# Kernel tuning notes

Hardware: AMD Instinct MI355X
Metric: run time of the kernel (lower is better)

The kernel has to match this reference:

```python
import jax, jax.numpy as jnp
import numpy as np

N_EMBD = 1024
N_HEAD = 16
HEAD_DIM = N_EMBD // N_HEAD
BLOCK = 2048
BATCH = 2


def setup_inputs() -> dict:
    key = jax.random.key(0)
    ks = jax.random.split(key, 6)
    s_in = 1.0 / np.sqrt(N_EMBD)
    s_hd = 1.0 / np.sqrt(N_EMBD)  # fan-in of c_proj1 is n_head*head_dim = n_embd
    return {
        "x": jax.random.normal(ks[0], (BATCH, BLOCK, N_EMBD), jnp.float32),
        "wq": jax.random.normal(ks[1], (N_EMBD, N_HEAD, HEAD_DIM), jnp.float32) * s_in,
        "wk": jax.random.normal(ks[2], (N_EMBD, N_HEAD, HEAD_DIM), jnp.float32) * s_in,
        "wv": jax.random.normal(ks[3], (N_EMBD, N_HEAD, HEAD_DIM), jnp.float32) * s_in,
        "wp1": jax.random.normal(ks[4], (N_HEAD, HEAD_DIM, N_EMBD), jnp.float32) * s_hd,
        "wp2": jax.random.normal(ks[5], (N_EMBD, N_EMBD), jnp.float32) * s_in,
    }


def reference(x, wq, wk, wv, wp1, wp2):
    # QKV projections: DenseGeneral(features=(H, D), axis=-1), no bias
    q = jnp.einsum('btc,chd->bthd', x, wq)
    k = jnp.einsum('btc,chd->bthd', x, wk)
    v = jnp.einsum('btc,chd->bthd', x, wv)
    scale = HEAD_DIM ** (-0.5)
    wei = jnp.einsum('bqhd,bkhd->bhqk', q, k) * scale  # [B,H,T,T]
    tril = jnp.tril(jnp.ones((BLOCK, BLOCK), dtype=bool))
    wei = jnp.where(tril, wei, -jnp.inf)
    wei = jax.nn.softmax(wei, axis=-1)
    att = jnp.einsum('bhqk,bkhd->bqhd', wei, v)  # [B,T,H,D]
    # c_proj1: DenseGeneral over (-2,-1) -> contract (H,D)
    y = jnp.einsum('bqhd,hdc->bqc', att, wp1)
    # c_proj2: Dense
    out = jnp.einsum('bqc,ce->bqe', y, wp2)
    return out
```

## Files before the change

### kernel.cpp

```cpp
#include <hip/hip_runtime.h>
#include <hip/hip_bf16.h>
#include <stdint.h>

typedef __bf16 bf16;
typedef __bf16 bf16x4 __attribute__((ext_vector_type(4)));
typedef __bf16 bf16x8 __attribute__((ext_vector_type(8)));
typedef float  f32x4  __attribute__((ext_vector_type(4)));

#define MFMA16(a,b,c) __builtin_amdgcn_mfma_f32_16x16x32_bf16((a),(b),(c),0,0,0)

#define TSEQ 2048
#define NE   1024
#define NE3  3072
#define NH   16
#define HD   64
#define MTOK 4096

#if defined(__has_builtin) && __has_builtin(__builtin_amdgcn_exp2f)
#define EXP2F(x) __builtin_amdgcn_exp2f(x)
#else
__device__ __forceinline__ float exp2_fast(float x) {
  float r; asm("v_exp_f32 %0, %1" : "=v"(r) : "v"(x)); return r;
}
#define EXP2F(x) exp2_fast(x)
#endif

__device__ __forceinline__ void gl_lds16(const bf16* g, bf16* l) {
  __builtin_amdgcn_global_load_lds(
      (const __attribute__((address_space(1))) void*)g,
      (__attribute__((address_space(3))) void*)l,
      16, 0, 0);
}

__global__ void k_cast(const float* __restrict__ in, bf16* __restrict__ out, int n4) {
  int i = blockIdx.x * blockDim.x + threadIdx.x;
  if (i < n4) {
    float4 v = reinterpret_cast<const float4*>(in)[i];
    bf16x4 o = { (bf16)v.x, (bf16)v.y, (bf16)v.z, (bf16)v.w };
    reinterpret_cast<bf16x4*>(out)[i] = o;
  }
}

__global__ void k_transpose_all(const float* __restrict__ wq, const float* __restrict__ wk,
                                const float* __restrict__ wv, const float* __restrict__ wp2,
                                const float* __restrict__ wp1,
                                bf16* __restrict__ W3T, bf16* __restrict__ Wp2T,
                                bf16* __restrict__ Wp1b) {
  __shared__ float tile[64][65];
  const int z = blockIdx.z;
  const int r0 = blockIdx.y * 64, c0 = blockIdx.x * 64;
  const int lc = threadIdx.x & 63, lr0 = threadIdx.x >> 6;
  if (z == 4) {
#pragma unroll
    for (int i = 0; i < 16; ++i) {
      int lr = i*4 + lr0;
      Wp1b[(size_t)(r0 + lr)*1024 + c0 + lc] = (bf16)wp1[(size_t)(r0 + lr)*1024 + c0 + lc];
    }
    return;
  }
  const float* in = (z == 0) ? wq : (z == 1) ? wk : (z == 2) ? wv : wp2;
  bf16* out = (z < 3) ? (W3T + (size_t)z * 1024 * 1024) : Wp2T;
#pragma unroll
  for (int i = 0; i < 16; ++i) {
    int lr = i*4 + lr0;
    tile[lr][lc] = in[(size_t)(r0 + lr) * 1024 + (c0 + lc)];
  }
  __syncthreads();
#pragma unroll
  for (int i = 0; i < 16; ++i) {
    int lr = i*4 + lr0;
    out[(size_t)(c0 + lr) * 1024 + (r0 + lc)] = (bf16)tile[lc][lr];
  }
}

__global__ void k_transpose_v(const bf16* __restrict__ V, bf16* __restrict__ Vt) {
  __shared__ bf16 tile[64][65];
  const int b = blockIdx.z, h = blockIdx.y, t0 = blockIdx.x * 64;
  const int lc = threadIdx.x & 63, lr0 = threadIdx.x >> 6;
#pragma unroll
  for (int i = 0; i < 16; ++i) {
    int lr = i*4 + lr0;
    tile[lr][lc] = V[(size_t)(b*TSEQ + t0 + lr)*NE3 + h*HD + lc];
  }
  __syncthreads();
#pragma unroll
  for (int i = 0; i < 16; ++i) {
    int lr = i*4 + lr0;
    Vt[((size_t)(b*NH + h)*HD + lr)*TSEQ + t0 + lc] = tile[lc][lr];
  }
}

template<int BN, typename OutT>
__global__ __launch_bounds__(256) void k_gemm_bt(const bf16* __restrict__ A,
                                                 const bf16* __restrict__ Bt,
                                                 OutT* __restrict__ C,
                                                 const int M, const int N, const int K) {
  constexpr int NC = BN / 32;
  __shared__ bf16 As[2][128*32];
  __shared__ bf16 Bs[2][BN*32];
  const int tid  = threadIdx.x;
  const int lane = tid & 63;
  const int wave = tid >> 6;
  const int wr = (wave >> 1) * 64;
  const int wc = (wave & 1) * (BN/2);
  const int l15 = lane & 15;
  const int l4  = lane >> 4;

  const int nwg = gridDim.x * gridDim.y;
  int id = blockIdx.y * gridDim.x + blockIdx.x;
  id = (id & 7) * (nwg >> 3) + (id >> 3);
  const int bm = (id / gridDim.x) * 128;
  const int bn = (id % gridDim.x) * BN;

  const int srow = tid >> 2;
  const int scol = ((tid & 3) ^ ((tid >> 3) & 3)) * 8;
  const bf16* ag = A  + (size_t)(bm + srow) * K + scol;
  const bf16* bg = Bt + (size_t)(bn + srow) * K + scol;
  const int kx = (l4 ^ ((l15 >> 1) & 3)) * 8;

  f32x4 acc[4][NC] = {};

  auto stage = [&](int buf, int k0) {
    bf16* al = As[buf] + tid * 8;
    bf16* bl = Bs[buf] + tid * 8;
    gl_lds16(ag + k0,                   al);
    gl_lds16(ag + k0 + (size_t)64 * K,  al + 64*32);
    gl_lds16(bg + k0,                   bl);
    if (BN == 128) gl_lds16(bg + k0 + (size_t)64 * K, bl + 64*32);
  };

  stage(0, 0);
  __syncthreads();
  int cur = 0;
  for (int k0 = 0; k0 < K; k0 += 32) {
    if (k0 + 32 < K) stage(cur ^ 1, k0 + 32);
    bf16x8 af[4], bfr[NC];
#pragma unroll
    for (int m = 0; m < 4; ++m)
      af[m] = *reinterpret_cast<const bf16x8*>(&As[cur][(wr + m*16 + l15)*32 + kx]);
#pragma unroll
    for (int n = 0; n < NC; ++n)
      bfr[n] = *reinterpret_cast<const bf16x8*>(&Bs[cur][(wc + n*16 + l15)*32 + kx]);
#pragma unroll
    for (int m = 0; m < 4; ++m)
#pragma unroll
      for (int n = 0; n < NC; ++n)
        acc[m][n] = MFMA16(af[m], bfr[n], acc[m][n]);
    __syncthreads();
    cur ^= 1;
  }

#pragma unroll
  for (int m = 0; m < 4; ++m) {
    const int row = bm + wr + m*16 + l4*4;
#pragma unroll
    for (int n = 0; n < NC; ++n) {
      const int col = bn + wc + n*16 + l15;
#pragma unroll
      for (int r = 0; r < 4; ++r)
        C[(size_t)(row + r) * N + col] = (OutT)acc[m][n][r];
    }
  }
}

__global__ __launch_bounds__(512) void k_attn(const bf16* __restrict__ QKV,
                                              const bf16* __restrict__ Vt,
                                              bf16* __restrict__ O) {
  __shared__ bf16 KVs[3][16384];
  __shared__ bf16 Ps[8][4*16*32];

  const int tid  = threadIdx.x;
  const int lane = tid & 63;
  const int wave = tid >> 6;
  const int l15 = lane & 15;
  const int l4  = lane >> 4;

  const int x  = blockIdx.x;
  const int p  = x >> 5;
  const int bh = x & 31;
  const int b  = bh >> 4, h = bh & 15;

  const bf16* Qb = QKV + (size_t)b*TSEQ*NE3 +        h*HD;
  const bf16* Kb = QKV + (size_t)b*TSEQ*NE3 + 1024 + h*HD;
  const bf16* Vb = Vt  + (size_t)bh*HD*TSEQ;
  bf16* Pw = Ps[wave];

  const float SC = 0.125f * 1.44269504f;
  const int swz = (l4 ^ ((l15 >> 1) & 3)) * 8;
  const int key = (l15 >> 1) & 3;

  const int krow = tid >> 2;
  const int kg   = (tid & 3) ^ ((krow >> 1) & 3);
  const int vd   = (tid >> 2) & 63;
  const int vg   = (tid & 3) ^ ((vd >> 1) & 3);
  const int vp0  = tid >> 8;

  auto tileOf = [&](int j) { return (j <= p) ? j : (j - p - 1); };

  auto stage = [&](int buf, int t) {
    bf16* kb = &KVs[buf][0];
    bf16* vb = &KVs[buf][8192];
#pragma unroll
    for (int kk = 0; kk < 2; ++kk)
      gl_lds16(&Kb[(size_t)(t*128 + krow)*NE3 + kk*32 + kg*8], kb + kk*4096 + tid*8);
#pragma unroll
    for (int kk = 0; kk < 2; ++kk) {
      const int ksv = kk*2 + vp0;
      gl_lds16(&Vb[(size_t)vd*TSEQ + t*128 + ksv*32 + vg*8],  vb + kk*4096 + tid*8);
    }
  };

  stage(0, tileOf(0));
  stage(1, tileOf(1));
  int i = 0;

  for (int ci = 0; ci < 2; ++ci) {
    const int c  = ci ? (15 - p) : p;
    const int qw = c*128 + wave*16;

    bf16x8 qf[2];
#pragma unroll
    for (int ks = 0; ks < 2; ++ks) {
      bf16x8 qv = *reinterpret_cast<const bf16x8*>(
          &Qb[(size_t)(qw + l15)*NE3 + ks*32 + l4*8]);
#pragma unroll
      for (int j = 0; j < 8; ++j) qv[j] = (bf16)((float)qv[j] * SC);
      qf[ks] = qv;
    }

    f32x4 ot[4] = {};
    float m_run = -1e30f;
    float l_part = 0.f;

    for (int t = 0; t <= c; ++t, ++i) {
      asm volatile("s_waitcnt vmcnt(4)" ::: "memory");
      __builtin_amdgcn_sched_barrier(0);
      __builtin_amdgcn_s_barrier();
      __builtin_amdgcn_sched_barrier(0);
      const int j2 = (i + 2 <= 16) ? (i + 2) : 16;
      stage((i + 2) % 3, tileOf(j2));
      __builtin_amdgcn_sched_barrier(0);

      const bf16* kbuf = &KVs[i % 3][0];
      const bf16* vbuf = &KVs[i % 3][8192];

      f32x4 st[8];
#pragma unroll
      for (int kvf = 0; kvf < 8; ++kvf) {
        st[kvf] = f32x4{0.f, 0.f, 0.f, 0.f};
        const int row = kvf*16 + l15;
#pragma unroll
        for (int ks = 0; ks < 2; ++ks) {
          bf16x8 kf = *reinterpret_cast<const bf16x8*>(&kbuf[ks*4096 + row*32 + swz]);
          st[kvf] = MFMA16(kf, qf[ks], st[kvf]);
        }
      }

      if (t == c) {
#pragma unroll
        for (int kvf = 0; kvf < 8; ++kvf)
#pragma unroll
          for (int r = 0; r < 4; ++r)
            if (kvf*16 + l4*4 + r > wave*16 + l15) st[kvf][r] = -1e30f;
      }

      float mx = st[0][0];
#pragma unroll
      for (int kvf = 0; kvf < 8; ++kvf)
#pragma unroll
        for (int r = 0; r < 4; ++r) mx = fmaxf(mx, st[kvf][r]);
      mx = fmaxf(mx, __shfl_xor(mx, 16));
      mx = fmaxf(mx, __shfl_xor(mx, 32));

      if (__any(mx > m_run + 8.f)) {
        const float mnew = fmaxf(m_run, mx);
        const float corr = EXP2F(m_run - mnew);
        l_part *= corr;
#pragma unroll
        for (int n2 = 0; n2 < 4; ++n2) ot[n2] *= corr;
        m_run = mnew;
      }

      float rs = 0.f;
#pragma unroll
      for (int kvf = 0; kvf < 8; ++kvf) {
        bf16x4 pk;
#pragma unroll
        for (int r = 0; r < 4; ++r) {
          const float pv = EXP2F(st[kvf][r] - m_run);
          rs += pv;
          pk[r] = (bf16)pv;
        }
        const int gp = (((kvf & 1)*2 + (l4 >> 1)) ^ key);
        *reinterpret_cast<bf16x4*>(
            &Pw[(kvf>>1)*512 + l15*32 + gp*8 + (l4 & 1)*4]) = pk;
      }
      l_part += rs;

      bf16x8 pa[4];
#pragma unroll
      for (int ksv = 0; ksv < 4; ++ksv)
        pa[ksv] = *reinterpret_cast<const bf16x8*>(&Pw[ksv*512 + l15*32 + swz]);
#pragma unroll
      for (int n2 = 0; n2 < 4; ++n2) {
        const int vrow = n2*16 + l15;
#pragma unroll
        for (int ksv = 0; ksv < 4; ++ksv) {
          bf16x8 vf = *reinterpret_cast<const bf16x8*>(&vbuf[ksv*2048 + vrow*32 + swz]);
          ot[n2] = MFMA16(vf, pa[ksv], ot[n2]);
        }
      }
    }

    float l = l_part;
    l += __shfl_xor(l, 16);
    l += __shfl_xor(l, 32);
    const float rl = 1.f / l;
    const size_t row = (size_t)(b*TSEQ + qw + l15);
#pragma unroll
    for (int n2 = 0; n2 < 4; ++n2) {
      bf16x4 ov;
#pragma unroll
      for (int r = 0; r < 4; ++r) ov[r] = (bf16)(ot[n2][r] * rl);
      *reinterpret_cast<bf16x4*>(&O[row*NE + h*HD + n2*16 + l4*4]) = ov;
    }
  }
}

extern "C" void kernel_launch(void* const* d_in, const int* in_sizes, int n_in,
                              void* d_out, int out_size, void* d_ws, size_t ws_size,
                              hipStream_t stream) {
  const float* x   = (const float*)d_in[0];
  const float* wq  = (const float*)d_in[1];
  const float* wk  = (const float*)d_in[2];
  const float* wv  = (const float*)d_in[3];
  const float* wp1 = (const float*)d_in[4];
  const float* wp2 = (const float*)d_in[5];
  float* out = (float*)d_out;

  char* ws = (char*)d_ws;
  const size_t MB = 1024ull * 1024ull;
  bf16* xb   = (bf16*)(ws + 0*MB);
  bf16* W3T  = (bf16*)(ws + 8*MB);
  bf16* wp1b = (bf16*)(ws + 14*MB);
  bf16* wp2T = (bf16*)(ws + 16*MB);
  bf16* WcT  = (bf16*)(ws + 18*MB);
  bf16* QKVb = (bf16*)(ws + 20*MB);
  bf16* Vtb  = (bf16*)(ws + 44*MB);
  bf16* attb = (bf16*)(ws + 52*MB);

  k_cast<<<4096, 256, 0, stream>>>(x, xb, MTOK*NE/4);
  k_transpose_all<<<dim3(16, 16, 5), 256, 0, stream>>>(wq, wk, wv, wp2, wp1,
                                                       W3T, wp2T, wp1b);

  k_gemm_bt<64, bf16><<<dim3(16, 8), 256, 0, stream>>>(wp2T, wp1b, WcT, 1024, 1024, 1024);

  k_gemm_bt<128, bf16><<<dim3(24, 32), 256, 0, stream>>>(xb, W3T, QKVb, MTOK, NE3, NE);

  k_transpose_v<<<dim3(TSEQ/64, NH, 2), 256, 0, stream>>>(QKVb + 2048, Vtb);

  k_attn<<<dim3(256), 512, 0, stream>>>(QKVb, Vtb, attb);

  k_gemm_bt<128, float><<<dim3(8, 32), 256, 0, stream>>>(attb, WcT, out, MTOK, NE, NE);
}
```

Measured before the change: 129.5 us.

## Rewrite attention with 32x32 MFMA, register-resident P via permlane swap

The attention kernel moves from 16x16x32 to 32x32x16 bf16 MFMA with 4 waves of 32 query rows each, instead of 8 waves of 16. Softmax probabilities are now packed with v_cvt_pk_bf16 and rearranged across lanes with v_permlane32_swap, so they feed the PV MFMA straight from registers instead of going through an LDS scratch buffer. It also skips fully masked key blocks on the diagonal tile and changes the K/V LDS swizzle to match the new layout. This removes LDS traffic and some masked work, but halves the waves per block and raises register pressure.

```diff
diff --git a/kernel.cpp b/kernel.cpp
--- a/kernel.cpp
+++ b/kernel.cpp
@@ -6,8 +6,10 @@
 typedef __bf16 bf16x4 __attribute__((ext_vector_type(4)));
 typedef __bf16 bf16x8 __attribute__((ext_vector_type(8)));
 typedef float  f32x4  __attribute__((ext_vector_type(4)));
+typedef float  f32x16 __attribute__((ext_vector_type(16)));
 
 #define MFMA16(a,b,c) __builtin_amdgcn_mfma_f32_16x16x32_bf16((a),(b),(c),0,0,0)
+#define MFMA32(a,b,c) __builtin_amdgcn_mfma_f32_32x32x16_bf16((a),(b),(c),0,0,0)
 
 #define TSEQ 2048
 #define NE   1024
@@ -24,6 +26,15 @@
 }
 #define EXP2F(x) exp2_fast(x)
 #endif
+
+__device__ __forceinline__ unsigned cvt_pk_bf16(float lo, float hi) {
+  unsigned r;
+  asm("v_cvt_pk_bf16_f32 %0, %1, %2" : "=v"(r) : "v"(lo), "v"(hi));
+  return r;
+}
+__device__ __forceinline__ void permlane32_swap(unsigned& a, unsigned& b) {
+  asm("v_permlane32_swap_b32 %0, %1" : "+v"(a), "+v"(b));
+}
 
 __device__ __forceinline__ void gl_lds16(const bf16* g, bf16* l) {
   __builtin_amdgcn_global_load_lds(
@@ -163,17 +174,16 @@
   }
 }
 
-__global__ __launch_bounds__(512) void k_attn(const bf16* __restrict__ QKV,
+__global__ __launch_bounds__(256) void k_attn(const bf16* __restrict__ QKV,
                                               const bf16* __restrict__ Vt,
                                               bf16* __restrict__ O) {
   __shared__ bf16 KVs[3][16384];
-  __shared__ bf16 Ps[8][4*16*32];
 
   const int tid  = threadIdx.x;
   const int lane = tid & 63;
   const int wave = tid >> 6;
-  const int l15 = lane & 15;
-  const int l4  = lane >> 4;
+  const int l31 = lane & 31;
+  const int l32 = lane >> 5;
 
   const int x  = blockIdx.x;
   const int p  = x >> 5;
@@ -183,17 +193,13 @@
   const bf16* Qb = QKV + (size_t)b*TSEQ*NE3 +        h*HD;
   const bf16* Kb = QKV + (size_t)b*TSEQ*NE3 + 1024 + h*HD;
   const bf16* Vb = Vt  + (size_t)bh*HD*TSEQ;
-  bf16* Pw = Ps[wave];
 
   const float SC = 0.125f * 1.44269504f;
-  const int swz = (l4 ^ ((l15 >> 1) & 3)) * 8;
-  const int key = (l15 >> 1) & 3;
-
-  const int krow = tid >> 2;
-  const int kg   = (tid & 3) ^ ((krow >> 1) & 3);
-  const int vd   = (tid >> 2) & 63;
-  const int vg   = (tid & 3) ^ ((vd >> 1) & 3);
-  const int vp0  = tid >> 8;
+
+  const int krow0 = tid >> 3;
+  const int kgd   = tid & 7;
+  const int vrow0 = tid >> 4;
+  const int vgd   = tid & 15;
 
   auto tileOf = [&](int j) { return (j <= p) ? j : (j - p - 1); };
 
@@ -201,12 +207,16 @@
     bf16* kb = &KVs[buf][0];
     bf16* vb = &KVs[buf][8192];
 #pragma unroll
-    for (int kk = 0; kk < 2; ++kk)
-      gl_lds16(&Kb[(size_t)(t*128 + krow)*NE3 + kk*32 + kg*8], kb + kk*4096 + tid*8);
-#pragma unroll
-    for (int kk = 0; kk < 2; ++kk) {
-      const int ksv = kk*2 + vp0;
-      gl_lds16(&Vb[(size_t)vd*TSEQ + t*128 + ksv*32 + vg*8],  vb + kk*4096 + tid*8);
+    for (int rr = 0; rr < 4; ++rr) {
+      const int r = rr*32 + krow0;
+      const int gs = kgd ^ (r & 7);
+      gl_lds16(&Kb[(size_t)(t*128 + r)*NE3 + gs*8], kb + rr*2048 + tid*8);
+    }
+#pragma unroll
+    for (int rr = 0; rr < 4; ++rr) {
+      const int d = rr*16 + vrow0;
+      const int gs = vgd ^ (d & 15);
+      gl_lds16(&Vb[(size_t)d*TSEQ + t*128 + gs*8], vb + rr*2048 + tid*8);
     }
   };
 
@@ -216,24 +226,24 @@
 
   for (int ci = 0; ci < 2; ++ci) {
     const int c  = ci ? (15 - p) : p;
-    const int qw = c*128 + wave*16;
-
-    bf16x8 qf[2];
-#pragma unroll
-    for (int ks = 0; ks < 2; ++ks) {
+    const int qw = c*128 + wave*32;
+
+    bf16x8 qf[4];
+#pragma unroll
+    for (int ks = 0; ks < 4; ++ks) {
       bf16x8 qv = *reinterpret_cast<const bf16x8*>(
-          &Qb[(size_t)(qw + l15)*NE3 + ks*32 + l4*8]);
+          &Qb[(size_t)(qw + l31)*NE3 + ks*16 + l32*8]);
 #pragma unroll
       for (int j = 0; j < 8; ++j) qv[j] = (bf16)((float)qv[j] * SC);
       qf[ks] = qv;
     }
 
-    f32x4 ot[4] = {};
+    f32x16 ot[2] = {};
     float m_run = -1e30f;
     float l_part = 0.f;
 
     for (int t = 0; t <= c; ++t, ++i) {
-      asm volatile("s_waitcnt vmcnt(4)" ::: "memory");
+      asm volatile("s_waitcnt vmcnt(8)" ::: "memory");
       __builtin_amdgcn_sched_barrier(0);
       __builtin_amdgcn_s_barrier();
       __builtin_amdgcn_sched_barrier(0);
@@ -244,32 +254,38 @@
       const bf16* kbuf = &KVs[i % 3][0];
       const bf16* vbuf = &KVs[i % 3][8192];
 
-      f32x4 st[8];
-#pragma unroll
-      for (int kvf = 0; kvf < 8; ++kvf) {
-        st[kvf] = f32x4{0.f, 0.f, 0.f, 0.f};
-        const int row = kvf*16 + l15;
-#pragma unroll
-        for (int ks = 0; ks < 2; ++ks) {
-          bf16x8 kf = *reinterpret_cast<const bf16x8*>(&kbuf[ks*4096 + row*32 + swz]);
-          st[kvf] = MFMA16(kf, qf[ks], st[kvf]);
+      const int nkb = (t == c) ? (wave + 1) : 4;
+
+      f32x16 st[4];
+#pragma unroll
+      for (int kb = 0; kb < 4; ++kb) {
+        if (kb >= nkb) continue;
+        f32x16 acc = {};
+        const int rk = kb*32 + l31;
+#pragma unroll
+        for (int ks = 0; ks < 4; ++ks) {
+          const int g = (2*ks + l32) ^ (rk & 7);
+          bf16x8 kf = *reinterpret_cast<const bf16x8*>(&kbuf[rk*64 + g*8]);
+          acc = MFMA32(kf, qf[ks], acc);
         }
+        st[kb] = acc;
       }
 
       if (t == c) {
 #pragma unroll
-        for (int kvf = 0; kvf < 8; ++kvf)
-#pragma unroll
-          for (int r = 0; r < 4; ++r)
-            if (kvf*16 + l4*4 + r > wave*16 + l15) st[kvf][r] = -1e30f;
-      }
-
-      float mx = st[0][0];
-#pragma unroll
-      for (int kvf = 0; kvf < 8; ++kvf)
-#pragma unroll
-        for (int r = 0; r < 4; ++r) mx = fmaxf(mx, st[kvf][r]);
-      mx = fmaxf(mx, __shfl_xor(mx, 16));
+        for (int r = 0; r < 16; ++r) {
+          const int o = (r & 3) + 8*(r >> 2) + 4*l32;
+          if (o > l31) st[wave][r] = -1e30f;
+        }
+      }
+
+      float mx = -1e30f;
+#pragma unroll
+      for (int kb = 0; kb < 4; ++kb) {
+        if (kb >= nkb) continue;
+#pragma unroll
+        for (int r = 0; r < 16; ++r) mx = fmaxf(mx, st[kb][r]);
+      }
       mx = fmaxf(mx, __shfl_xor(mx, 32));
 
       if (__any(mx > m_run + 8.f)) {
@@ -277,53 +293,67 @@
         const float corr = EXP2F(m_run - mnew);
         l_part *= corr;
 #pragma unroll
-        for (int n2 = 0; n2 < 4; ++n2) ot[n2] *= corr;
+        for (int dbl = 0; dbl < 2; ++dbl) ot[dbl] *= corr;
         m_run = mnew;
       }
 
-      float rs = 0.f;
-#pragma unroll
-      for (int kvf = 0; kvf < 8; ++kvf) {
-        bf16x4 pk;
-#pragma unroll
-        for (int r = 0; r < 4; ++r) {
-          const float pv = EXP2F(st[kvf][r] - m_run);
-          rs += pv;
-          pk[r] = (bf16)pv;
+      bf16x8 pb[8];
+#pragma unroll
+      for (int kb = 0; kb < 4; ++kb) {
+        if (kb >= nkb) continue;
+        float pv[16];
+#pragma unroll
+        for (int r = 0; r < 16; ++r) {
+          pv[r] = EXP2F(st[kb][r] - m_run);
+          l_part += pv[r];
         }
-        const int gp = (((kvf & 1)*2 + (l4 >> 1)) ^ key);
-        *reinterpret_cast<bf16x4*>(
-            &Pw[(kvf>>1)*512 + l15*32 + gp*8 + (l4 & 1)*4]) = pk;
-      }
-      l_part += rs;
-
-      bf16x8 pa[4];
-#pragma unroll
-      for (int ksv = 0; ksv < 4; ++ksv)
-        pa[ksv] = *reinterpret_cast<const bf16x8*>(&Pw[ksv*512 + l15*32 + swz]);
-#pragma unroll
-      for (int n2 = 0; n2 < 4; ++n2) {
-        const int vrow = n2*16 + l15;
-#pragma unroll
-        for (int ksv = 0; ksv < 4; ++ksv) {
-          bf16x8 vf = *reinterpret_cast<const bf16x8*>(&vbuf[ksv*2048 + vrow*32 + swz]);
-          ot[n2] = MFMA16(vf, pa[ksv], ot[n2]);
+        unsigned c01 = cvt_pk_bf16(pv[0],  pv[1]);
+        unsigned c23 = cvt_pk_bf16(pv[2],  pv[3]);
+        unsigned c45 = cvt_pk_bf16(pv[4],  pv[5]);
+        unsigned c67 = cvt_pk_bf16(pv[6],  pv[7]);
+        unsigned c89 = cvt_pk_bf16(pv[8],  pv[9]);
+        unsigned cAB = cvt_pk_bf16(pv[10], pv[11]);
+        unsigned cCD = cvt_pk_bf16(pv[12], pv[13]);
+        unsigned cEF = cvt_pk_bf16(pv[14], pv[15]);
+        permlane32_swap(c01, c45);
+        permlane32_swap(c23, c67);
+        permlane32_swap(c89, cCD);
+        permlane32_swap(cAB, cEF);
+        union { unsigned u[4]; bf16x8 v; } f0, f1;
+        f0.u[0] = c01; f0.u[1] = c23; f0.u[2] = c45; f0.u[3] = c67;
+        f1.u[0] = c89; f1.u[1] = cAB; f1.u[2] = cCD; f1.u[3] = cEF;
+        pb[2*kb]     = f0.v;
+        pb[2*kb + 1] = f1.v;
+      }
+
+#pragma unroll
+      for (int dbl = 0; dbl < 2; ++dbl) {
+        const int d = dbl*32 + l31;
+        f32x16 acc = ot[dbl];
+#pragma unroll
+        for (int ksv = 0; ksv < 8; ++ksv) {
+          if (ksv >= 2*nkb) continue;
+          const int g = (2*ksv + l32) ^ (d & 15);
+          bf16x8 vf = *reinterpret_cast<const bf16x8*>(&vbuf[d*128 + g*8]);
+          acc = MFMA32(vf, pb[ksv], acc);
         }
-      }
-    }
-
-    float l = l_part;
-    l += __shfl_xor(l, 16);
-    l += __shfl_xor(l, 32);
+        ot[dbl] = acc;
+      }
+    }
+
+    float l = l_part + __shfl_xor(l_part, 32);
     const float rl = 1.f / l;
-    const size_t row = (size_t)(b*TSEQ + qw + l15);
-#pragma unroll
-    for (int n2 = 0; n2 < 4; ++n2) {
-      bf16x4 ov;
-#pragma unroll
-      for (int r = 0; r < 4; ++r) ov[r] = (bf16)(ot[n2][r] * rl);
-      *reinterpret_cast<bf16x4*>(&O[row*NE + h*HD + n2*16 + l4*4]) = ov;
-    }
+    const size_t row = (size_t)(b*TSEQ + qw + l31);
+#pragma unroll
+    for (int dbl = 0; dbl < 2; ++dbl)
+#pragma unroll
+      for (int u = 0; u < 4; ++u) {
+        const int d0 = dbl*32 + u*8 + 4*l32;
+        bf16x4 ov;
+#pragma unroll
+        for (int v = 0; v < 4; ++v) ov[v] = (bf16)(ot[dbl][u*4 + v] * rl);
+        *reinterpret_cast<bf16x4*>(&O[row*NE + h*HD + d0]) = ov;
+      }
   }
 }
 
@@ -359,7 +389,7 @@
 
   k_transpose_v<<<dim3(TSEQ/64, NH, 2), 256, 0, stream>>>(QKVb + 2048, Vtb);
 
-  k_attn<<<dim3(256), 512, 0, stream>>>(QKVb, Vtb, attb);
+  k_attn<<<dim3(256), 256, 0, stream>>>(QKVb, Vtb, attb);
 
   k_gemm_bt<128, float><<<dim3(8, 32), 256, 0, stream>>>(attb, WcT, out, MTOK, NE, NE);
 }
```

Result: slower. 191.4 us (+47.8%).
